# Kernel optimization log

Hardware: AMD Instinct MI355X
Metric: run time of the kernel (lower is better)

## Reference

```python
import jax, jax.numpy as jnp
import numpy as np

D = 128  # node_state_dim
T = 8    # message-passing steps
FEAT = 26


def _dense_relu(x, W, b):
    return jax.nn.relu(x @ W + b)


def _gru(x, h, k, rk, bi, br):
    # Keras GRUCell (reset_after=True) math, inference (no dropout).
    xz, xr, xh = jnp.split(x @ k + bi, 3, axis=-1)
    hz, hr, hh = jnp.split(h @ rk + br, 3, axis=-1)
    z = jax.nn.sigmoid(xz + hz)
    r = jax.nn.sigmoid(xr + hr)
    hcand = jnp.tanh(xh + r * hh)
    return z * h + (1.0 - z) * hcand


def _segment_mean(data, ids, num_segments):
    s = jax.ops.segment_sum(data, ids, num_segments=num_segments)
    cnt = jax.ops.segment_sum(jnp.ones((data.shape[0],), data.dtype), ids,
                              num_segments=num_segments)
    return jnp.where(cnt[:, None] > 0, s / jnp.maximum(cnt, 1.0)[:, None], 0.0)


def setup_inputs() -> dict:
    key = jax.random.key(0)
    ks = jax.random.split(key, 24)
    n_i, n_c, n_e = 50000, 100000, 200000
    glorot = lambda k, shape: jax.random.normal(k, shape, jnp.float32) * np.sqrt(2.0 / (shape[0] + shape[1]))
    inp = {
        'feature_connection': jax.random.normal(ks[0], (n_c, FEAT), jnp.float32),
        'src_ip_to_connection': jax.random.randint(ks[1], (n_e,), 0, n_i),
        'dst_ip_to_connection': jax.random.randint(ks[2], (n_e,), 0, n_c),
        'src_connection_to_ip': jax.random.randint(ks[3], (n_e,), 0, n_c),
        'dst_connection_to_ip': jax.random.randint(ks[4], (n_e,), 0, n_i),
        'n_i': n_i, 'n_c': n_c,
        # message MLPs: Dense(2D -> D)
        'Wm1': glorot(ks[5], (2 * D, D)), 'bm1': jnp.zeros((D,), jnp.float32),
        'Wm2': glorot(ks[6], (2 * D, D)), 'bm2': jnp.zeros((D,), jnp.float32),
        # GRU cells: kernel [D,3D], recurrent_kernel [D,3D], input/recurrent biases [3D]
        'k_ip': glorot(ks[7], (D, 3 * D)), 'rk_ip': glorot(ks[8], (D, 3 * D)),
        'bi_ip': jnp.zeros((3 * D,), jnp.float32), 'br_ip': jnp.zeros((3 * D,), jnp.float32),
        'k_conn': glorot(ks[9], (D, 3 * D)), 'rk_conn': glorot(ks[10], (D, 3 * D)),
        'bi_conn': jnp.zeros((3 * D,), jnp.float32), 'br_conn': jnp.zeros((3 * D,), jnp.float32),
        # readout: D -> 128 -> 64 -> 15 softmax
        'Wr1': glorot(ks[11], (D, 128)), 'br1': jnp.zeros((128,), jnp.float32),
        'Wr2': glorot(ks[12], (128, 64)), 'br2': jnp.zeros((64,), jnp.float32),
        'Wr3': glorot(ks[13], (64, 15)), 'br3': jnp.zeros((15,), jnp.float32),
    }
    return inp


def reference(feature_connection, src_ip_to_connection, dst_ip_to_connection,
              src_connection_to_ip, dst_connection_to_ip, n_i, n_c,
              Wm1, bm1, Wm2, bm2,
              k_ip, rk_ip, bi_ip, br_ip,
              k_conn, rk_conn, bi_conn, br_conn,
              Wr1, br1, Wr2, br2, Wr3, br3):
    ip_state = jnp.ones((n_i, D), jnp.float32)
    connection_state = jnp.concatenate(
        [feature_connection, jnp.zeros((n_c, D - FEAT), jnp.float32)], axis=1)

    def step(carry, _):
        ip_state, connection_state = carry
        # ip -> connection messages
        nn_in1 = jnp.concatenate([ip_state[src_ip_to_connection],
                                  connection_state[dst_ip_to_connection]], axis=1)
        ip_message = _dense_relu(nn_in1, Wm1, bm1)
        ip_mean = _segment_mean(ip_message, dst_ip_to_connection, n_c)
        # connection -> ip messages
        nn_in2 = jnp.concatenate([connection_state[src_connection_to_ip],
                                  ip_state[dst_connection_to_ip]], axis=1)
        conn_message = _dense_relu(nn_in2, Wm2, bm2)
        conn_mean = _segment_mean(conn_message, dst_connection_to_ip, n_i)
        ip_state = _gru(conn_mean, ip_state, k_ip, rk_ip, bi_ip, br_ip)
        connection_state = _gru(ip_mean, connection_state, k_conn, rk_conn, bi_conn, br_conn)
        return (ip_state, connection_state), None

    (ip_state, connection_state), _ = jax.lax.scan(step, (ip_state, connection_state),
                                                   None, length=T)
    h = _dense_relu(connection_state, Wr1, br1)
    h = _dense_relu(h, Wr2, br2)
    return jax.nn.softmax(h @ Wr3 + br3, axis=-1)
```

## Files before the change

### kernel.cpp

```cpp
#include <hip/hip_runtime.h>
#include <math.h>

#define D 128
#define T_STEPS 8
#define FEAT 26

typedef short bf16x8 __attribute__((ext_vector_type(8)));
typedef unsigned short u16x8 __attribute__((ext_vector_type(8)));
typedef float f32x4 __attribute__((ext_vector_type(4)));

__device__ inline unsigned short f2bf(float f) {
    unsigned b = __float_as_uint(f);
    b += 0x7FFFu + ((b >> 16) & 1u);
    return (unsigned short)(b >> 16);
}
__device__ inline float bf2f(unsigned short u) {
    return __uint_as_float(((unsigned)u) << 16);
}

__device__ inline void gl_lds16(const void* g, void* l) {
    __builtin_amdgcn_global_load_lds(
        (const __attribute__((address_space(1))) void*)g,
        (__attribute__((address_space(3))) void*)l, 16, 0, 0);
}

__device__ inline float fast_sigmoid(float x) {
    float e = __builtin_amdgcn_exp2f(-1.442695041f * x);
    return __builtin_amdgcn_rcpf(1.0f + e);
}
__device__ inline float fast_tanh(float x) {
    float e = __builtin_amdgcn_exp2f(2.885390082f * x);
    return 1.0f - 2.0f * __builtin_amdgcn_rcpf(1.0f + e);
}

__global__ void k_init_ip(unsigned short* __restrict__ ip_state, int n) {
    int i = blockIdx.x * blockDim.x + threadIdx.x;
    if (i < n) ip_state[i] = 0x3F80;
}

__global__ void k_init_conn(unsigned short* __restrict__ conn_state,
                            const float* __restrict__ feat, int n_c) {
    int i = blockIdx.x * blockDim.x + threadIdx.x;
    if (i < n_c * D) {
        int r = i >> 7;
        int d = i & 127;
        conn_state[i] = (d < FEAT) ? f2bf(feat[r * FEAT + d]) : (unsigned short)0;
    }
}

__global__ void k_wcat(const float* __restrict__ Wm1, const float* __restrict__ Wm2,
                       float* __restrict__ Wip, float* __restrict__ Wcn) {
    int i = blockIdx.x * blockDim.x + threadIdx.x;
    if (i < 128 * 256) {
        int k = i >> 8, j = i & 255;
        Wip[i] = (j < 128) ? Wm1[k * 128 + j] : Wm2[(128 + k) * 128 + (j - 128)];
        Wcn[i] = (j < 128) ? Wm2[k * 128 + j] : Wm1[(128 + k) * 128 + (j - 128)];
    }
}

__global__ void k_wstack512(const float* __restrict__ K, const float* __restrict__ RK,
                            float* __restrict__ W512) {
    int i = blockIdx.x * blockDim.x + threadIdx.x;
    if (i < 256 * 512) {
        int k = i >> 9, j = i & 511;
        float v = 0.f;
        if (k < 128) {
            if (j < 384) v = K[k * 384 + j];
        } else {
            if (j < 256) v = RK[(k - 128) * 384 + j];
            else if (j >= 384) v = RK[(k - 128) * 384 + (j - 128)];
        }
        W512[i] = v;
    }
}

__global__ void k_gbias(const float* __restrict__ bi, const float* __restrict__ br,
                        float* __restrict__ cb) {
    int d = threadIdx.x;
    cb[d] = bi[d] + br[d];
    cb[128 + d] = bi[128 + d] + br[128 + d];
    cb[256 + d] = bi[256 + d];
    cb[384 + d] = br[256 + d];
}

__global__ void k_pack1(const float* __restrict__ Wf, short* __restrict__ WG,
                        int ksteps, int nct, int N) {
    int id = blockIdx.x * blockDim.x + threadIdx.x;
    int total = ksteps * nct * 512;
    if (id < total) {
        int i = id & 7;
        int l = (id >> 3) & 63;
        int rest = id >> 9;
        int q = rest % nct;
        int s = rest / nct;
        int k = s * 32 + (l >> 4) * 8 + i;
        int col = q * 16 + (l & 15);
        float f = Wf[(size_t)k * N + col];
        unsigned b = __float_as_uint(f);
        b += 0x7FFFu + ((b >> 16) & 1u);
        WG[id] = (short)(b >> 16);
    }
}

__global__ void k_pack_gru1(const float* __restrict__ W512, short* __restrict__ WG) {
    int id = blockIdx.x * blockDim.x + threadIdx.x;
    int total = 8 * 24 * 512;
    if (id < total) {
        int i = id & 7;
        int l = (id >> 3) & 63;
        int rest = id >> 9;
        int q = rest % 24;
        int s = rest / 24;
        int ct = (s < 4) ? q : (q < 16 ? q : q + 8);
        int k = s * 32 + (l >> 4) * 8 + i;
        int col = ct * 16 + (l & 15);
        float f = W512[(size_t)k * 512 + col];
        unsigned b = __float_as_uint(f);
        b += 0x7FFFu + ((b >> 16) & 1u);
        WG[id] = (short)(b >> 16);
    }
}

__global__ void k_counts(const int* __restrict__ dst_a, const int* __restrict__ dst_b,
                         int* __restrict__ cnt_c, int* __restrict__ cnt_i, int n_e) {
    int i = blockIdx.x * blockDim.x + threadIdx.x;
    if (i < n_e) {
        atomicAdd(&cnt_c[dst_a[i]], 1);
        atomicAdd(&cnt_i[dst_b[i]], 1);
    }
}

__global__ void k_scan1(const int* __restrict__ cnt, int* __restrict__ off,
                        int* __restrict__ bsum, int n) {
    __shared__ int wsh[4];
    int tid = threadIdx.x, lane = tid & 63, wid = tid >> 6;
    int base = blockIdx.x * 2048 + tid * 8;
    int v[8], pref[8];
    int s = 0;
#pragma unroll
    for (int j = 0; j < 8; ++j) {
        v[j] = (base + j < n) ? cnt[base + j] : 0;
        pref[j] = s; s += v[j];
    }
    int x = s;
#pragma unroll
    for (int o = 1; o < 64; o <<= 1) {
        int y = __shfl_up(x, o, 64);
        if (lane >= o) x += y;
    }
    if (lane == 63) wsh[wid] = x;
    __syncthreads();
    int wbase = 0, tot = 0;
#pragma unroll
    for (int w = 0; w < 4; ++w) { if (w < wid) wbase += wsh[w]; tot += wsh[w]; }
    int tbase = wbase + (x - s);
#pragma unroll
    for (int j = 0; j < 8; ++j)
        if (base + j < n) off[base + j] = tbase + pref[j];
    if (tid == 0) bsum[blockIdx.x] = tot;
}

__global__ void k_scan2(int* __restrict__ bsum, int nb) {
    __shared__ int wsh[4];
    int tid = threadIdx.x, lane = tid & 63, wid = tid >> 6;
    int v = (tid < nb) ? bsum[tid] : 0;
    int x = v;
#pragma unroll
    for (int o = 1; o < 64; o <<= 1) {
        int y = __shfl_up(x, o, 64);
        if (lane >= o) x += y;
    }
    if (lane == 63) wsh[wid] = x;
    __syncthreads();
    int wbase = 0;
#pragma unroll
    for (int w = 0; w < 4; ++w) if (w < wid) wbase += wsh[w];
    if (tid < nb) bsum[tid] = wbase + (x - v);
}

__global__ void k_scan3(int* __restrict__ off, const int* __restrict__ bsum, int n) {
    int i = blockIdx.x * blockDim.x + threadIdx.x;
    if (i < n) off[i] += bsum[i >> 11];
}

__global__ void k_scatter(const int* __restrict__ dst, const int* __restrict__ src,
                          const int* __restrict__ off, int* __restrict__ cursor,
                          int* __restrict__ elist, int n_e) {
    int i = blockIdx.x * blockDim.x + threadIdx.x;
    if (i < n_e) {
        int d = dst[i];
        int pos = off[d] + atomicAdd(&cursor[d], 1);
        elist[pos] = src[i];
    }
}

template <int KSTEPS, int NCT, int EPI, int OUTBF>
__global__ __launch_bounds__(256, 4) void k_mgemm9_dual(
    const unsigned short* __restrict__ S0, const unsigned short* __restrict__ S1,
    int sstride,
    const short* __restrict__ WG0, const short* __restrict__ WG1,
    const float* __restrict__ bias,
    void* __restrict__ O0, void* __restrict__ O1, int ostride,
    int nblk0, int n0, int n1)
{
    constexpr int NQW = NCT / 2;
    constexpr int PHU = NCT * 64;
    __shared__ short lw[2][PHU * 8];
    int b = blockIdx.x;
    bool sec = b >= nblk0;
    const unsigned short* S = sec ? S1 : S0;
    const short* WG = sec ? WG1 : WG0;
    void* OUT = sec ? O1 : O0;
    int n = sec ? n1 : n0;
    int r0 = (sec ? b - nblk0 : b) * 64;

    int tid = threadIdx.x;
    int l = tid & 63, w = tid >> 6;
    int rt = w >> 1, cg = w & 1;
    int g = l >> 4, ln = l & 15;
    int rb = r0 + rt * 32;
    int rowc0 = rb + ln;      if (rowc0 >= n) rowc0 = n - 1;
    int rowc1 = rb + 16 + ln; if (rowc1 >= n) rowc1 = n - 1;

    bf16x8 u0[KSTEPS], u1[KSTEPS];
#pragma unroll
    for (int s = 0; s < KSTEPS; ++s) {
        u0[s] = *(const bf16x8*)&S[(size_t)rowc0 * sstride + s * 32 + g * 8];
        u1[s] = *(const bf16x8*)&S[(size_t)rowc1 * sstride + s * 32 + g * 8];
    }

    f32x4 acc0[NQW], acc1[NQW];
#pragma unroll
    for (int c = 0; c < NQW; ++c) {
        acc0[c] = (f32x4){0.f, 0.f, 0.f, 0.f};
        acc1[c] = (f32x4){0.f, 0.f, 0.f, 0.f};
    }

#pragma unroll
    for (int t = 0; t < PHU / 256; ++t)
        gl_lds16(WG + ((size_t)(t * 256 + tid)) * 8,
                 &lw[0][(size_t)(t * 256 + w * 64) * 8]);
    __syncthreads();

#pragma unroll
    for (int s = 0; s < KSTEPS; ++s) {
        if (s + 1 < KSTEPS) {
#pragma unroll
            for (int t = 0; t < PHU / 256; ++t)
                gl_lds16(WG + ((size_t)(s + 1) * PHU + t * 256 + tid) * 8,
                         &lw[(s + 1) & 1][(size_t)(t * 256 + w * 64) * 8]);
        }
        const short* lb = lw[s & 1];
#pragma unroll
        for (int c = 0; c < NQW; ++c) {
            int q = cg * NQW + c;
            bf16x8 wv = *(const bf16x8*)&lb[((size_t)q * 64 + l) * 8];
            acc0[c] = __builtin_amdgcn_mfma_f32_16x16x32_bf16(u0[s], wv, acc0[c], 0, 0, 0);
            acc1[c] = __builtin_amdgcn_mfma_f32_16x16x32_bf16(u1[s], wv, acc1[c], 0, 0, 0);
        }
        __syncthreads();
    }

#pragma unroll
    for (int c = 0; c < NQW; ++c) {
        int col = (cg * NQW + c) * 16 + ln;
        float bv = (EPI == 1) ? bias[col] : 0.f;
#pragma unroll
        for (int i = 0; i < 4; ++i) {
            int gr0 = rb + g * 4 + i;
            int gr1 = gr0 + 16;
            float v0 = acc0[c][i], v1 = acc1[c][i];
            if (EPI == 1) { v0 = fmaxf(v0 + bv, 0.f); v1 = fmaxf(v1 + bv, 0.f); }
            if (OUTBF == 1) {
                unsigned short* O = (unsigned short*)OUT;
                if (gr0 < n) O[(size_t)gr0 * ostride + col] = f2bf(v0);
                if (gr1 < n) O[(size_t)gr1 * ostride + col] = f2bf(v1);
            } else {
                float* O = (float*)OUT;
                if (gr0 < n) O[(size_t)gr0 * ostride + col] = v0;
                if (gr1 < n) O[(size_t)gr1 * ostride + col] = v1;
            }
        }
    }
}

__global__ __launch_bounds__(256, 2) void k_gru11_dual(
    const unsigned short* __restrict__ P0, const unsigned short* __restrict__ Q0,
    const int* __restrict__ el0, const int* __restrict__ of0,
    const int* __restrict__ ct0, const float* __restrict__ mb0,
    unsigned short* __restrict__ H0, const short* __restrict__ WGa,
    const float* __restrict__ cba,
    const unsigned short* __restrict__ P1, const unsigned short* __restrict__ Q1,
    const int* __restrict__ el1, const int* __restrict__ of1,
    const int* __restrict__ ct1, const float* __restrict__ mb1,
    unsigned short* __restrict__ H1, const short* __restrict__ WGb,
    const float* __restrict__ cbb,
    int nblk0, int n0, int n1)
{
    constexpr int PHU1 = 24 * 64;
    __shared__ short lw[2 * PHU1 * 8];
    __shared__ unsigned short xs[64][136];
    int b = blockIdx.x;
    bool sec = b >= nblk0;
    const unsigned short* Pother = sec ? P1 : P0;
    const unsigned short* Qown   = sec ? Q1 : Q0;
    const int* elist = sec ? el1 : el0;
    const int* off   = sec ? of1 : of0;
    const int* cnt   = sec ? ct1 : ct0;
    const float* mb  = sec ? mb1 : mb0;
    unsigned short* state = sec ? H1 : H0;
    const short* WG = sec ? WGb : WGa;
    const float* cb = sec ? cbb : cba;
    int n = sec ? n1 : n0;
    int r0 = (sec ? b - nblk0 : b) * 64;

    int tid = threadIdx.x;
    int l = tid & 63, w = tid >> 6;
    int rt = w >> 1, cg = w & 1;
    int g = l >> 4, ln = l & 15;
    int rb = r0 + rt * 32;

    {
        int lr = tid >> 2;
        int cq = (tid & 3) * 32;
        int node = r0 + lr; if (node >= n) node = n - 1;
        int deg = cnt[node];
        float av[32];
#pragma unroll
        for (int k = 0; k < 32; ++k) av[k] = 0.f;
        if (deg > 0) {
            int o = off[node];
            float qvf[32];
#pragma unroll
            for (int jj = 0; jj < 4; ++jj) {
                u16x8 qv8 = *(const u16x8*)&Qown[(size_t)node * 256 + cq + jj * 8];
#pragma unroll
                for (int k = 0; k < 8; ++k)
                    qvf[jj * 8 + k] = bf2f(qv8[k]) + mb[cq + jj * 8 + k];
            }
            for (int e = 0; e < deg; ++e) {
                int sidx = elist[o + e];
                const unsigned short* prow = Pother + (size_t)sidx * 256 + cq;
#pragma unroll
                for (int jj = 0; jj < 4; ++jj) {
                    u16x8 pv = *(const u16x8*)&prow[jj * 8];
#pragma unroll
                    for (int k = 0; k < 8; ++k)
                        av[jj * 8 + k] += fmaxf(bf2f(pv[k]) + qvf[jj * 8 + k], 0.f);
                }
            }
            float inv = 1.0f / (float)deg;
#pragma unroll
            for (int k = 0; k < 32; ++k) av[k] *= inv;
        }
#pragma unroll
        for (int jj = 0; jj < 4; ++jj) {
            u16x8 o8;
#pragma unroll
            for (int k = 0; k < 8; ++k) o8[k] = f2bf(av[jj * 8 + k]);
            *(u16x8*)&xs[lr][cq + jj * 8] = o8;
        }
    }
    __syncthreads();

    int lrow0 = rt * 32 + ln;
    int lrow1 = lrow0 + 16;
    bf16x8 u0[4], u1[4];
#pragma unroll
    for (int ss = 0; ss < 4; ++ss) {
        u0[ss] = *(const bf16x8*)&xs[lrow0][ss * 32 + g * 8];
        u1[ss] = *(const bf16x8*)&xs[lrow1][ss * 32 + g * 8];
    }
    __syncthreads();

    f32x4 acc0[16], acc1[16];
#pragma unroll
    for (int c = 0; c < 16; ++c) {
        acc0[c] = (f32x4){0.f, 0.f, 0.f, 0.f};
        acc1[c] = (f32x4){0.f, 0.f, 0.f, 0.f};
    }

#pragma unroll
    for (int p = 0; p < 4; ++p) {
#pragma unroll
        for (int t = 0; t < 12; ++t)
            gl_lds16(WG + ((size_t)p * 2 * PHU1 + t * 256 + tid) * 8,
                     &lw[(size_t)(t * 256 + w * 64) * 8]);
        if (p == 2) {
#pragma unroll
            for (int i = 0; i < 4; ++i) {
                int id = i * 256 + tid;
                int r = id >> 4, c8 = id & 15;
                int gr = r0 + r; if (gr >= n) gr = n - 1;
                *(u16x8*)&xs[r][c8 * 8] =
                    *(const u16x8*)&state[(size_t)gr * 128 + c8 * 8];
            }
        }
        __syncthreads();
        if (p == 2) {
#pragma unroll
            for (int s2 = 0; s2 < 4; ++s2) {
                u0[s2] = *(const bf16x8*)&xs[lrow0][s2 * 32 + g * 8];
                u1[s2] = *(const bf16x8*)&xs[lrow1][s2 * 32 + g * 8];
            }
        }
#pragma unroll
        for (int sub = 0; sub < 2; ++sub) {
            const int s = p * 2 + sub;
            const int ss = s & 3;
            const short* lb = lw + (size_t)sub * PHU1 * 8;
#pragma unroll
            for (int jp = 0; jp < 4; ++jp) {
                int qz = cg * 4 + jp;
                int qr = 8 + cg * 4 + jp;
                int qh = 16 + cg * 4 + jp;
                int aih = (s < 4) ? (8 + jp) : (12 + jp);
#define PROC(Q, AI) do {                                                        \
                bf16x8 wv = *(const bf16x8*)&lb[(((size_t)(Q)) * 64 + l) * 8];  \
                acc0[AI] = __builtin_amdgcn_mfma_f32_16x16x32_bf16(u0[ss], wv, acc0[AI], 0, 0, 0); \
                acc1[AI] = __builtin_amdgcn_mfma_f32_16x16x32_bf16(u1[ss], wv, acc1[AI], 0, 0, 0); \
            } while (0)
                PROC(qz, jp);
                PROC(qr, 4 + jp);
                PROC(qh, aih);
#undef PROC
            }
        }
        if (p + 1 < 4) __syncthreads();
    }

#pragma unroll
    for (int jp = 0; jp < 4; ++jp) {
        int d = (cg * 4 + jp) * 16 + ln;
        float bz = cb[d], brr = cb[128 + d], bxh = cb[256 + d], bhh = cb[384 + d];
#pragma unroll
        for (int rs = 0; rs < 2; ++rs) {
            f32x4 az = rs ? acc1[jp] : acc0[jp];
            f32x4 ar = rs ? acc1[4 + jp] : acc0[4 + jp];
            f32x4 axh = rs ? acc1[8 + jp] : acc0[8 + jp];
            f32x4 ahh = rs ? acc1[12 + jp] : acc0[12 + jp];
#pragma unroll
            for (int i = 0; i < 4; ++i) {
                int lr = rt * 32 + rs * 16 + g * 4 + i;
                int gr = r0 + lr;
                if (gr < n) {
                    float h = bf2f(xs[lr][d]);
                    float z = fast_sigmoid(az[i] + bz);
                    float r = fast_sigmoid(ar[i] + brr);
                    float hc = fast_tanh(axh[i] + bxh + r * (ahh[i] + bhh));
                    state[(size_t)gr * 128 + d] = f2bf(z * h + (1.0f - z) * hc);
                }
            }
        }
    }
}

__global__ __launch_bounds__(256) void k_read2(
    const float* __restrict__ h1,
    const float* __restrict__ W2, const float* __restrict__ b2,
    const float* __restrict__ W3, const float* __restrict__ b3,
    float* __restrict__ out, int n)
{
    __shared__ float W2ls[128][64];
    __shared__ float W3ls[64][16];
    __shared__ float h1ls[8][132];
    __shared__ float h2ls[8][66];
    __shared__ float lgls[8][16];
    int tid = threadIdx.x;
    int r0 = blockIdx.x * 8;

#pragma unroll
    for (int i = 0; i < 8; ++i) {
        int id = i * 256 + tid;
        int kr = id >> 4, c4 = id & 15;
        *(float4*)&W2ls[kr][c4 * 4] = *(const float4*)&W2[kr * 64 + c4 * 4];
    }
    for (int id = tid; id < 960; id += 256) {
        W3ls[id / 15][id % 15] = W3[id];
    }
    {
        int r = tid >> 5, c4 = tid & 31;
        int gr = r0 + r; if (gr >= n) gr = n - 1;
        *(float4*)&h1ls[r][c4 * 4] = *(const float4*)&h1[(size_t)gr * 128 + c4 * 4];
    }
    __syncthreads();

    {
        int row = tid >> 5, c = tid & 31;
        float a0 = b2[c], a1 = b2[c + 32];
        for (int k = 0; k < 128; ++k) {
            float h = h1ls[row][k];
            a0 = fmaf(h, W2ls[k][c], a0);
            a1 = fmaf(h, W2ls[k][c + 32], a1);
        }
        h2ls[row][c] = fmaxf(a0, 0.f);
        h2ls[row][c + 32] = fmaxf(a1, 0.f);
    }
    __syncthreads();

    if (tid < 120) {
        int row = tid / 15, c = tid % 15;
        float a = b3[c];
        for (int k = 0; k < 64; ++k) a = fmaf(h2ls[row][k], W3ls[k][c], a);
        lgls[row][c] = a;
    }
    __syncthreads();

    if (tid < 120) {
        int row = tid / 15, c = tid % 15;
        int gr = r0 + row;
        if (gr < n) {
            float m = -1e30f;
#pragma unroll
            for (int k = 0; k < 15; ++k) m = fmaxf(m, lgls[row][k]);
            float s = 0.f;
#pragma unroll
            for (int k = 0; k < 15; ++k) s += expf(lgls[row][k] - m);
            out[(size_t)gr * 15 + c] = expf(lgls[row][c] - m) / s;
        }
    }
}

extern "C" void kernel_launch(void* const* d_in, const int* in_sizes, int n_in,
                              void* d_out, int out_size, void* d_ws, size_t ws_size,
                              hipStream_t stream) {
    const float* feat   = (const float*)d_in[0];
    const int*   src_ip = (const int*)d_in[1];
    const int*   dst_ip = (const int*)d_in[2];
    const int*   src_cn = (const int*)d_in[3];
    const int*   dst_cn = (const int*)d_in[4];
    const float* Wm1 = (const float*)d_in[7];
    const float* bm1 = (const float*)d_in[8];
    const float* Wm2 = (const float*)d_in[9];
    const float* bm2 = (const float*)d_in[10];
    const float* k_ip  = (const float*)d_in[11];
    const float* rk_ip = (const float*)d_in[12];
    const float* bi_ip = (const float*)d_in[13];
    const float* br_ip = (const float*)d_in[14];
    const float* k_cn  = (const float*)d_in[15];
    const float* rk_cn = (const float*)d_in[16];
    const float* bi_cn = (const float*)d_in[17];
    const float* br_cn = (const float*)d_in[18];
    const float* Wr1 = (const float*)d_in[19];
    const float* br1 = (const float*)d_in[20];
    const float* Wr2 = (const float*)d_in[21];
    const float* br2 = (const float*)d_in[22];
    const float* Wr3 = (const float*)d_in[23];
    const float* br3 = (const float*)d_in[24];

    const int n_e = in_sizes[1];
    const int n_c = in_sizes[0] / FEAT;
    const int n_i = 50000;

    auto align = [](size_t x) { return (x + 255) & ~(size_t)255; };
    char* ws = (char*)d_ws;
    size_t off = 0;
    unsigned short* ip_state   = (unsigned short*)(ws + off); off = align(off + (size_t)n_i * D * 2);
    unsigned short* conn_state = (unsigned short*)(ws + off); off = align(off + (size_t)n_c * D * 2);
    unsigned short* PQ_ip = (unsigned short*)(ws + off); off = align(off + (size_t)n_i * 256 * 2);
    unsigned short* PQ_cn = (unsigned short*)(ws + off); off = align(off + (size_t)n_c * 256 * 2);
    float* h1buf      = (float*)(ws + off); off = align(off + (size_t)n_c * 128 * 4);
    float* Wip        = (float*)(ws + off); off = align(off + (size_t)128 * 256 * 4);
    float* Wcn        = (float*)(ws + off); off = align(off + (size_t)128 * 256 * 4);
    float* W512f      = (float*)(ws + off); off = align(off + (size_t)256 * 512 * 4);
    short* WGpq_ip    = (short*)(ws + off); off = align(off + (size_t)4 * 16 * 512 * 2);
    short* WGpq_cn    = (short*)(ws + off); off = align(off + (size_t)4 * 16 * 512 * 2);
    short* WGg_ip     = (short*)(ws + off); off = align(off + (size_t)8 * 24 * 512 * 2);
    short* WGg_cn     = (short*)(ws + off); off = align(off + (size_t)8 * 24 * 512 * 2);
    short* WGr1       = (short*)(ws + off); off = align(off + (size_t)4 * 8 * 512 * 2);
    float* cb_ip      = (float*)(ws + off); off = align(off + (size_t)512 * 4);
    float* cb_cn      = (float*)(ws + off); off = align(off + (size_t)512 * 4);
    int*   cnt_c      = (int*)(ws + off);   off = align(off + (size_t)n_c * 4);
    int*   cnt_i      = (int*)(ws + off);   off = align(off + (size_t)n_i * 4);
    int*   off_c      = (int*)(ws + off);   off = align(off + (size_t)n_c * 4);
    int*   off_i      = (int*)(ws + off);   off = align(off + (size_t)n_i * 4);
    int*   cursor     = (int*)(ws + off);   off = align(off + (size_t)n_c * 4);
    int*   elist_c    = (int*)(ws + off);   off = align(off + (size_t)n_e * 4);
    int*   elist_i    = (int*)(ws + off);   off = align(off + (size_t)n_e * 4);
    int*   bsum_c     = (int*)(ws + off);   off = align(off + (size_t)64 * 4);
    int*   bsum_i     = (int*)(ws + off);   off = align(off + (size_t)64 * 4);

    k_init_ip<<<(n_i * D + 255) / 256, 256, 0, stream>>>(ip_state, n_i * D);
    k_init_conn<<<(n_c * D + 255) / 256, 256, 0, stream>>>(conn_state, feat, n_c);

    k_wcat<<<(128 * 256 + 255) / 256, 256, 0, stream>>>(Wm1, Wm2, Wip, Wcn);
    k_pack1<<<(4 * 16 * 512 + 255) / 256, 256, 0, stream>>>(Wip, WGpq_ip, 4, 16, 256);
    k_pack1<<<(4 * 16 * 512 + 255) / 256, 256, 0, stream>>>(Wcn, WGpq_cn, 4, 16, 256);
    k_wstack512<<<(256 * 512 + 255) / 256, 256, 0, stream>>>(k_ip, rk_ip, W512f);
    k_pack_gru1<<<(8 * 24 * 512 + 255) / 256, 256, 0, stream>>>(W512f, WGg_ip);
    k_wstack512<<<(256 * 512 + 255) / 256, 256, 0, stream>>>(k_cn, rk_cn, W512f);
    k_pack_gru1<<<(8 * 24 * 512 + 255) / 256, 256, 0, stream>>>(W512f, WGg_cn);
    k_pack1<<<(4 * 8 * 512 + 255) / 256, 256, 0, stream>>>(Wr1, WGr1, 4, 8, 128);
    k_gbias<<<1, 128, 0, stream>>>(bi_ip, br_ip, cb_ip);
    k_gbias<<<1, 128, 0, stream>>>(bi_cn, br_cn, cb_cn);

    hipMemsetAsync(cnt_c, 0, (size_t)n_c * 4, stream);
    hipMemsetAsync(cnt_i, 0, (size_t)n_i * 4, stream);
    k_counts<<<(n_e + 255) / 256, 256, 0, stream>>>(dst_ip, dst_cn, cnt_c, cnt_i, n_e);
    int nb_c = (n_c + 2047) / 2048, nb_i = (n_i + 2047) / 2048;
    k_scan1<<<nb_c, 256, 0, stream>>>(cnt_c, off_c, bsum_c, n_c);
    k_scan1<<<nb_i, 256, 0, stream>>>(cnt_i, off_i, bsum_i, n_i);
    k_scan2<<<1, 256, 0, stream>>>(bsum_c, nb_c);
    k_scan2<<<1, 256, 0, stream>>>(bsum_i, nb_i);
    k_scan3<<<(n_c + 255) / 256, 256, 0, stream>>>(off_c, bsum_c, n_c);
    k_scan3<<<(n_i + 255) / 256, 256, 0, stream>>>(off_i, bsum_i, n_i);
    hipMemsetAsync(cursor, 0, (size_t)n_c * 4, stream);
    k_scatter<<<(n_e + 255) / 256, 256, 0, stream>>>(dst_ip, src_ip, off_c, cursor, elist_c, n_e);
    hipMemsetAsync(cursor, 0, (size_t)n_c * 4, stream);
    k_scatter<<<(n_e + 255) / 256, 256, 0, stream>>>(dst_cn, src_cn, off_i, cursor, elist_i, n_e);

    int b64_i = (n_i + 63) / 64;
    int b64_c = (n_c + 63) / 64;

    for (int t = 0; t < T_STEPS; ++t) {
        k_mgemm9_dual<4, 16, 0, 1><<<b64_i + b64_c, 256, 0, stream>>>(
            ip_state, conn_state, 128, WGpq_ip, WGpq_cn, nullptr,
            PQ_ip, PQ_cn, 256, b64_i, n_i, n_c);
        k_gru11_dual<<<b64_i + b64_c, 256, 0, stream>>>(
            PQ_cn, PQ_ip + 128, elist_i, off_i, cnt_i, bm2, ip_state, WGg_ip, cb_ip,
            PQ_ip, PQ_cn + 128, elist_c, off_c, cnt_c, bm1, conn_state, WGg_cn, cb_cn,
            b64_i, n_i, n_c);
    }

    k_mgemm9_dual<4, 8, 1, 0><<<b64_c, 256, 0, stream>>>(
        conn_state, conn_state, 128, WGr1, WGr1, br1,
        h1buf, h1buf, 128, b64_c, n_c, n_c);
    k_read2<<<(n_c + 7) / 8, 256, 0, stream>>>(
        h1buf, Wr2, br2, Wr3, br3, (float*)d_out, n_c);
}
```

Before: 1.341 ms.

## Merge setup kernels into dual launches and hoist weight LDS prefetch earlier

Fuses the paired preprocessing kernels (state init, weight packing, bias, scans, scatter) into single dual-dispatch launches. It also drops the intermediate fp32 weight buffers and collapses the memsets into one zero-fill with separate cursors. In the GEMM and GRU kernels, the phase-0 weight copy to LDS is issued before state loads to overlap with them, removing one barrier. The goal is to cut launch count and serialization overhead in setup and to hide weight-load latency. The cost is more complex indexing, with a risk of LDS hazards now that a __syncthreads is removed.

```diff
diff --git a/kernel.cpp b/kernel.cpp
--- a/kernel.cpp
+++ b/kernel.cpp
@@ -33,49 +33,27 @@
     return 1.0f - 2.0f * __builtin_amdgcn_rcpf(1.0f + e);
 }
 
-__global__ void k_init_ip(unsigned short* __restrict__ ip_state, int n) {
+__global__ void k_init_dual(unsigned short* __restrict__ ip_state,
+                            unsigned short* __restrict__ conn_state,
+                            const float* __restrict__ feat, int ni_elems,
+                            int total) {
     int i = blockIdx.x * blockDim.x + threadIdx.x;
-    if (i < n) ip_state[i] = 0x3F80;
-}
-
-__global__ void k_init_conn(unsigned short* __restrict__ conn_state,
-                            const float* __restrict__ feat, int n_c) {
-    int i = blockIdx.x * blockDim.x + threadIdx.x;
-    if (i < n_c * D) {
-        int r = i >> 7;
-        int d = i & 127;
-        conn_state[i] = (d < FEAT) ? f2bf(feat[r * FEAT + d]) : (unsigned short)0;
-    }
-}
-
-__global__ void k_wcat(const float* __restrict__ Wm1, const float* __restrict__ Wm2,
-                       float* __restrict__ Wip, float* __restrict__ Wcn) {
-    int i = blockIdx.x * blockDim.x + threadIdx.x;
-    if (i < 128 * 256) {
-        int k = i >> 8, j = i & 255;
-        Wip[i] = (j < 128) ? Wm1[k * 128 + j] : Wm2[(128 + k) * 128 + (j - 128)];
-        Wcn[i] = (j < 128) ? Wm2[k * 128 + j] : Wm1[(128 + k) * 128 + (j - 128)];
-    }
-}
-
-__global__ void k_wstack512(const float* __restrict__ K, const float* __restrict__ RK,
-                            float* __restrict__ W512) {
-    int i = blockIdx.x * blockDim.x + threadIdx.x;
-    if (i < 256 * 512) {
-        int k = i >> 9, j = i & 511;
-        float v = 0.f;
-        if (k < 128) {
-            if (j < 384) v = K[k * 384 + j];
-        } else {
-            if (j < 256) v = RK[(k - 128) * 384 + j];
-            else if (j >= 384) v = RK[(k - 128) * 384 + (j - 128)];
-        }
-        W512[i] = v;
-    }
-}
-
-__global__ void k_gbias(const float* __restrict__ bi, const float* __restrict__ br,
-                        float* __restrict__ cb) {
+    if (i < ni_elems) {
+        ip_state[i] = 0x3F80;
+    } else if (i < total) {
+        int j = i - ni_elems;
+        int r = j >> 7, d = j & 127;
+        conn_state[j] = (d < FEAT) ? f2bf(feat[r * FEAT + d]) : (unsigned short)0;
+    }
+}
+
+__global__ void k_gbias_dual(const float* __restrict__ bi0, const float* __restrict__ br0,
+                             float* __restrict__ cb0,
+                             const float* __restrict__ bi1, const float* __restrict__ br1,
+                             float* __restrict__ cb1) {
+    const float* bi = blockIdx.x ? bi1 : bi0;
+    const float* br = blockIdx.x ? br1 : br0;
+    float* cb = blockIdx.x ? cb1 : cb0;
     int d = threadIdx.x;
     cb[d] = bi[d] + br[d];
     cb[128 + d] = bi[128 + d] + br[128 + d];
@@ -83,28 +61,35 @@
     cb[384 + d] = br[256 + d];
 }
 
-__global__ void k_pack1(const float* __restrict__ Wf, short* __restrict__ WG,
-                        int ksteps, int nct, int N) {
+__global__ void k_pack_pq_dual(const float* __restrict__ Wm1,
+                               const float* __restrict__ Wm2,
+                               short* __restrict__ WGip, short* __restrict__ WGcn) {
     int id = blockIdx.x * blockDim.x + threadIdx.x;
-    int total = ksteps * nct * 512;
-    if (id < total) {
+    if (id < 4 * 16 * 512) {
         int i = id & 7;
         int l = (id >> 3) & 63;
         int rest = id >> 9;
-        int q = rest % nct;
-        int s = rest / nct;
+        int q = rest % 16;
+        int s = rest / 16;
         int k = s * 32 + (l >> 4) * 8 + i;
         int col = q * 16 + (l & 15);
-        float f = Wf[(size_t)k * N + col];
-        unsigned b = __float_as_uint(f);
-        b += 0x7FFFu + ((b >> 16) & 1u);
-        WG[id] = (short)(b >> 16);
-    }
-}
-
-__global__ void k_pack_gru1(const float* __restrict__ W512, short* __restrict__ WG) {
-    int id = blockIdx.x * blockDim.x + threadIdx.x;
+        float fip = (col < 128) ? Wm1[k * 128 + col] : Wm2[(128 + k) * 128 + (col - 128)];
+        float fcn = (col < 128) ? Wm2[k * 128 + col] : Wm1[(128 + k) * 128 + (col - 128)];
+        WGip[id] = (short)f2bf(fip);
+        WGcn[id] = (short)f2bf(fcn);
+    }
+}
+
+__global__ void k_pack_gru_dual(const float* __restrict__ K0, const float* __restrict__ RK0,
+                                short* __restrict__ WG0,
+                                const float* __restrict__ K1, const float* __restrict__ RK1,
+                                short* __restrict__ WG1, int nblk0) {
     int total = 8 * 24 * 512;
+    bool sec = blockIdx.x >= nblk0;
+    const float* K = sec ? K1 : K0;
+    const float* RK = sec ? RK1 : RK0;
+    short* WG = sec ? WG1 : WG0;
+    int id = (sec ? blockIdx.x - nblk0 : blockIdx.x) * blockDim.x + threadIdx.x;
     if (id < total) {
         int i = id & 7;
         int l = (id >> 3) & 63;
@@ -114,10 +99,29 @@
         int ct = (s < 4) ? q : (q < 16 ? q : q + 8);
         int k = s * 32 + (l >> 4) * 8 + i;
         int col = ct * 16 + (l & 15);
-        float f = W512[(size_t)k * 512 + col];
-        unsigned b = __float_as_uint(f);
-        b += 0x7FFFu + ((b >> 16) & 1u);
-        WG[id] = (short)(b >> 16);
+        float v = 0.f;
+        if (k < 128) {
+            if (col < 384) v = K[k * 384 + col];
+        } else {
+            int kk = k - 128;
+            if (col < 256) v = RK[kk * 384 + col];
+            else if (col >= 384) v = RK[kk * 384 + (col - 128)];
+        }
+        WG[id] = (short)f2bf(v);
+    }
+}
+
+__global__ void k_pack_r1(const float* __restrict__ Wf, short* __restrict__ WG) {
+    int id = blockIdx.x * blockDim.x + threadIdx.x;
+    if (id < 4 * 8 * 512) {
+        int i = id & 7;
+        int l = (id >> 3) & 63;
+        int rest = id >> 9;
+        int q = rest % 8;
+        int s = rest / 8;
+        int k = s * 32 + (l >> 4) * 8 + i;
+        int col = q * 16 + (l & 15);
+        WG[id] = (short)f2bf(Wf[(size_t)k * 128 + col]);
     }
 }
 
@@ -130,11 +134,10 @@
     }
 }
 
-__global__ void k_scan1(const int* __restrict__ cnt, int* __restrict__ off,
-                        int* __restrict__ bsum, int n) {
+__device__ inline void scan1_body(const int* cnt, int* off, int* bsum, int n, int blk) {
     __shared__ int wsh[4];
     int tid = threadIdx.x, lane = tid & 63, wid = tid >> 6;
-    int base = blockIdx.x * 2048 + tid * 8;
+    int base = blk * 2048 + tid * 8;
     int v[8], pref[8];
     int s = 0;
 #pragma unroll
@@ -157,11 +160,22 @@
 #pragma unroll
     for (int j = 0; j < 8; ++j)
         if (base + j < n) off[base + j] = tbase + pref[j];
-    if (tid == 0) bsum[blockIdx.x] = tot;
-}
-
-__global__ void k_scan2(int* __restrict__ bsum, int nb) {
+    if (tid == 0) bsum[blk] = tot;
+}
+
+__global__ void k_scan1_dual(const int* __restrict__ cnt_c, int* __restrict__ off_c,
+                             int* __restrict__ bsum_c, int n_c, int nb_c,
+                             const int* __restrict__ cnt_i, int* __restrict__ off_i,
+                             int* __restrict__ bsum_i, int n_i) {
+    if ((int)blockIdx.x < nb_c) scan1_body(cnt_c, off_c, bsum_c, n_c, blockIdx.x);
+    else scan1_body(cnt_i, off_i, bsum_i, n_i, blockIdx.x - nb_c);
+}
+
+__global__ void k_scan2_dual(int* __restrict__ bsum_c, int nb_c,
+                             int* __restrict__ bsum_i, int nb_i) {
     __shared__ int wsh[4];
+    int* bsum = blockIdx.x ? bsum_i : bsum_c;
+    int nb = blockIdx.x ? nb_i : nb_c;
     int tid = threadIdx.x, lane = tid & 63, wid = tid >> 6;
     int v = (tid < nb) ? bsum[tid] : 0;
     int x = v;
@@ -178,15 +192,31 @@
     if (tid < nb) bsum[tid] = wbase + (x - v);
 }
 
-__global__ void k_scan3(int* __restrict__ off, const int* __restrict__ bsum, int n) {
+__global__ void k_scan3_dual(int* __restrict__ off_c, const int* __restrict__ bsum_c,
+                             int n_c,
+                             int* __restrict__ off_i, const int* __restrict__ bsum_i,
+                             int n_i) {
     int i = blockIdx.x * blockDim.x + threadIdx.x;
-    if (i < n) off[i] += bsum[i >> 11];
-}
-
-__global__ void k_scatter(const int* __restrict__ dst, const int* __restrict__ src,
-                          const int* __restrict__ off, int* __restrict__ cursor,
-                          int* __restrict__ elist, int n_e) {
-    int i = blockIdx.x * blockDim.x + threadIdx.x;
+    if (i < n_c) off_c[i] += bsum_c[i >> 11];
+    else if (i < n_c + n_i) {
+        int j = i - n_c;
+        off_i[j] += bsum_i[j >> 11];
+    }
+}
+
+__global__ void k_scatter_dual(
+    const int* __restrict__ dst0, const int* __restrict__ src0,
+    const int* __restrict__ off0, int* __restrict__ cur0, int* __restrict__ el0,
+    const int* __restrict__ dst1, const int* __restrict__ src1,
+    const int* __restrict__ off1, int* __restrict__ cur1, int* __restrict__ el1,
+    int n_e, int nb_e) {
+    bool sec = (int)blockIdx.x >= nb_e;
+    const int* dst = sec ? dst1 : dst0;
+    const int* src = sec ? src1 : src0;
+    const int* off = sec ? off1 : off0;
+    int* cursor = sec ? cur1 : cur0;
+    int* elist = sec ? el1 : el0;
+    int i = (sec ? blockIdx.x - nb_e : blockIdx.x) * blockDim.x + threadIdx.x;
     if (i < n_e) {
         int d = dst[i];
         int pos = off[d] + atomicAdd(&cursor[d], 1);
@@ -222,6 +252,11 @@
     int rowc0 = rb + ln;      if (rowc0 >= n) rowc0 = n - 1;
     int rowc1 = rb + 16 + ln; if (rowc1 >= n) rowc1 = n - 1;
 
+#pragma unroll
+    for (int t = 0; t < PHU / 256; ++t)
+        gl_lds16(WG + ((size_t)(t * 256 + tid)) * 8,
+                 &lw[0][(size_t)(t * 256 + w * 64) * 8]);
+
     bf16x8 u0[KSTEPS], u1[KSTEPS];
 #pragma unroll
     for (int s = 0; s < KSTEPS; ++s) {
@@ -235,11 +270,6 @@
         acc0[c] = (f32x4){0.f, 0.f, 0.f, 0.f};
         acc1[c] = (f32x4){0.f, 0.f, 0.f, 0.f};
     }
-
-#pragma unroll
-    for (int t = 0; t < PHU / 256; ++t)
-        gl_lds16(WG + ((size_t)(t * 256 + tid)) * 8,
-                 &lw[0][(size_t)(t * 256 + w * 64) * 8]);
     __syncthreads();
 
 #pragma unroll
@@ -320,6 +350,11 @@
     int g = l >> 4, ln = l & 15;
     int rb = r0 + rt * 32;
 
+#pragma unroll
+    for (int t = 0; t < 12; ++t)
+        gl_lds16(WG + ((size_t)(t * 256 + tid)) * 8,
+                 &lw[(size_t)(t * 256 + w * 64) * 8]);
+
     {
         int lr = tid >> 2;
         int cq = (tid & 3) * 32;
@@ -371,7 +406,6 @@
         u0[ss] = *(const bf16x8*)&xs[lrow0][ss * 32 + g * 8];
         u1[ss] = *(const bf16x8*)&xs[lrow1][ss * 32 + g * 8];
     }
-    __syncthreads();
 
     f32x4 acc0[16], acc1[16];
 #pragma unroll
@@ -382,26 +416,28 @@
 
 #pragma unroll
     for (int p = 0; p < 4; ++p) {
-#pragma unroll
-        for (int t = 0; t < 12; ++t)
-            gl_lds16(WG + ((size_t)p * 2 * PHU1 + t * 256 + tid) * 8,
-                     &lw[(size_t)(t * 256 + w * 64) * 8]);
-        if (p == 2) {
-#pragma unroll
-            for (int i = 0; i < 4; ++i) {
-                int id = i * 256 + tid;
-                int r = id >> 4, c8 = id & 15;
-                int gr = r0 + r; if (gr >= n) gr = n - 1;
-                *(u16x8*)&xs[r][c8 * 8] =
-                    *(const u16x8*)&state[(size_t)gr * 128 + c8 * 8];
+        if (p > 0) {
+#pragma unroll
+            for (int t = 0; t < 12; ++t)
+                gl_lds16(WG + ((size_t)p * 2 * PHU1 + t * 256 + tid) * 8,
+                         &lw[(size_t)(t * 256 + w * 64) * 8]);
+            if (p == 2) {
+#pragma unroll
+                for (int i = 0; i < 4; ++i) {
+                    int id = i * 256 + tid;
+                    int r = id >> 4, c8 = id & 15;
+                    int gr = r0 + r; if (gr >= n) gr = n - 1;
+                    *(u16x8*)&xs[r][c8 * 8] =
+                        *(const u16x8*)&state[(size_t)gr * 128 + c8 * 8];
+                }
             }
-        }
-        __syncthreads();
-        if (p == 2) {
-#pragma unroll
-            for (int s2 = 0; s2 < 4; ++s2) {
-                u0[s2] = *(const bf16x8*)&xs[lrow0][s2 * 32 + g * 8];
-                u1[s2] = *(const bf16x8*)&xs[lrow1][s2 * 32 + g * 8];
+            __syncthreads();
+            if (p == 2) {
+#pragma unroll
+                for (int s2 = 0; s2 < 4; ++s2) {
+                    u0[s2] = *(const bf16x8*)&xs[lrow0][s2 * 32 + g * 8];
+                    u1[s2] = *(const bf16x8*)&xs[lrow1][s2 * 32 + g * 8];
+                }
             }
         }
 #pragma unroll
@@ -560,9 +596,6 @@
     unsigned short* PQ_ip = (unsigned short*)(ws + off); off = align(off + (size_t)n_i * 256 * 2);
     unsigned short* PQ_cn = (unsigned short*)(ws + off); off = align(off + (size_t)n_c * 256 * 2);
     float* h1buf      = (float*)(ws + off); off = align(off + (size_t)n_c * 128 * 4);
-    float* Wip        = (float*)(ws + off); off = align(off + (size_t)128 * 256 * 4);
-    float* Wcn        = (float*)(ws + off); off = align(off + (size_t)128 * 256 * 4);
-    float* W512f      = (float*)(ws + off); off = align(off + (size_t)256 * 512 * 4);
     short* WGpq_ip    = (short*)(ws + off); off = align(off + (size_t)4 * 16 * 512 * 2);
     short* WGpq_cn    = (short*)(ws + off); off = align(off + (size_t)4 * 16 * 512 * 2);
     short* WGg_ip     = (short*)(ws + off); off = align(off + (size_t)8 * 24 * 512 * 2);
@@ -570,44 +603,46 @@
     short* WGr1       = (short*)(ws + off); off = align(off + (size_t)4 * 8 * 512 * 2);
     float* cb_ip      = (float*)(ws + off); off = align(off + (size_t)512 * 4);
     float* cb_cn      = (float*)(ws + off); off = align(off + (size_t)512 * 4);
-    int*   cnt_c      = (int*)(ws + off);   off = align(off + (size_t)n_c * 4);
-    int*   cnt_i      = (int*)(ws + off);   off = align(off + (size_t)n_i * 4);
+    int*   zb         = (int*)(ws + off);   off = align(off + (size_t)(2 * n_c + 2 * n_i) * 4);
+    int*   cnt_c      = zb;
+    int*   cnt_i      = zb + n_c;
+    int*   cursor_c   = zb + n_c + n_i;
+    int*   cursor_i   = zb + 2 * n_c + n_i;
     int*   off_c      = (int*)(ws + off);   off = align(off + (size_t)n_c * 4);
     int*   off_i      = (int*)(ws + off);   off = align(off + (size_t)n_i * 4);
-    int*   cursor     = (int*)(ws + off);   off = align(off + (size_t)n_c * 4);
     int*   elist_c    = (int*)(ws + off);   off = align(off + (size_t)n_e * 4);
     int*   elist_i    = (int*)(ws + off);   off = align(off + (size_t)n_e * 4);
     int*   bsum_c     = (int*)(ws + off);   off = align(off + (size_t)64 * 4);
     int*   bsum_i     = (int*)(ws + off);   off = align(off + (size_t)64 * 4);
 
-    k_init_ip<<<(n_i * D + 255) / 256, 256, 0, stream>>>(ip_state, n_i * D);
-    k_init_conn<<<(n_c * D + 255) / 256, 256, 0, stream>>>(conn_state, feat, n_c);
-
-    k_wcat<<<(128 * 256 + 255) / 256, 256, 0, stream>>>(Wm1, Wm2, Wip, Wcn);
-    k_pack1<<<(4 * 16 * 512 + 255) / 256, 256, 0, stream>>>(Wip, WGpq_ip, 4, 16, 256);
-    k_pack1<<<(4 * 16 * 512 + 255) / 256, 256, 0, stream>>>(Wcn, WGpq_cn, 4, 16, 256);
-    k_wstack512<<<(256 * 512 + 255) / 256, 256, 0, stream>>>(k_ip, rk_ip, W512f);
-    k_pack_gru1<<<(8 * 24 * 512 + 255) / 256, 256, 0, stream>>>(W512f, WGg_ip);
-    k_wstack512<<<(256 * 512 + 255) / 256, 256, 0, stream>>>(k_cn, rk_cn, W512f);
-    k_pack_gru1<<<(8 * 24 * 512 + 255) / 256, 256, 0, stream>>>(W512f, WGg_cn);
-    k_pack1<<<(4 * 8 * 512 + 255) / 256, 256, 0, stream>>>(Wr1, WGr1, 4, 8, 128);
-    k_gbias<<<1, 128, 0, stream>>>(bi_ip, br_ip, cb_ip);
-    k_gbias<<<1, 128, 0, stream>>>(bi_cn, br_cn, cb_cn);
-
-    hipMemsetAsync(cnt_c, 0, (size_t)n_c * 4, stream);
-    hipMemsetAsync(cnt_i, 0, (size_t)n_i * 4, stream);
+    int init_total = n_i * D + n_c * D;
+    k_init_dual<<<(init_total + 255) / 256, 256, 0, stream>>>(
+        ip_state, conn_state, feat, n_i * D, init_total);
+
+    k_pack_pq_dual<<<(4 * 16 * 512 + 255) / 256, 256, 0, stream>>>(
+        Wm1, Wm2, WGpq_ip, WGpq_cn);
+    {
+        int nbg = (8 * 24 * 512 + 255) / 256;
+        k_pack_gru_dual<<<2 * nbg, 256, 0, stream>>>(
+            k_ip, rk_ip, WGg_ip, k_cn, rk_cn, WGg_cn, nbg);
+    }
+    k_pack_r1<<<(4 * 8 * 512 + 255) / 256, 256, 0, stream>>>(Wr1, WGr1);
+    k_gbias_dual<<<2, 128, 0, stream>>>(bi_ip, br_ip, cb_ip, bi_cn, br_cn, cb_cn);
+
+    hipMemsetAsync(zb, 0, (size_t)(2 * n_c + 2 * n_i) * 4, stream);
     k_counts<<<(n_e + 255) / 256, 256, 0, stream>>>(dst_ip, dst_cn, cnt_c, cnt_i, n_e);
     int nb_c = (n_c + 2047) / 2048, nb_i = (n_i + 2047) / 2048;
-    k_scan1<<<nb_c, 256, 0, stream>>>(cnt_c, off_c, bsum_c, n_c);
-    k_scan1<<<nb_i, 256, 0, stream>>>(cnt_i, off_i, bsum_i, n_i);
-    k_scan2<<<1, 256, 0, stream>>>(bsum_c, nb_c);
-    k_scan2<<<1, 256, 0, stream>>>(bsum_i, nb_i);
-    k_scan3<<<(n_c + 255) / 256, 256, 0, stream>>>(off_c, bsum_c, n_c);
-    k_scan3<<<(n_i + 255) / 256, 256, 0, stream>>>(off_i, bsum_i, n_i);
-    hipMemsetAsync(cursor, 0, (size_t)n_c * 4, stream);
-    k_scatter<<<(n_e + 255) / 256, 256, 0, stream>>>(dst_ip, src_ip, off_c, cursor, elist_c, n_e);
-    hipMemsetAsync(cursor, 0, (size_t)n_c * 4, stream);
-    k_scatter<<<(n_e + 255) / 256, 256, 0, stream>>>(dst_cn, src_cn, off_i, cursor, elist_i, n_e);
+    k_scan1_dual<<<nb_c + nb_i, 256, 0, stream>>>(
+        cnt_c, off_c, bsum_c, n_c, nb_c, cnt_i, off_i, bsum_i, n_i);
+    k_scan2_dual<<<2, 256, 0, stream>>>(bsum_c, nb_c, bsum_i, nb_i);
+    k_scan3_dual<<<(n_c + n_i + 255) / 256, 256, 0, stream>>>(
+        off_c, bsum_c, n_c, off_i, bsum_i, n_i);
+    {
+        int nb_e = (n_e + 255) / 256;
+        k_scatter_dual<<<2 * nb_e, 256, 0, stream>>>(
+            dst_ip, src_ip, off_c, cursor_c, elist_c,
+            dst_cn, src_cn, off_i, cursor_i, elist_i, n_e, nb_e);
+    }
 
     int b64_i = (n_i + 63) / 64;
     int b64_c = (n_c + 63) / 64;
```

Measured after the change: 1.291 ms. -3.8%, faster.
